# Optimization experiments

Hardware: AMD Instinct MI355X
Metric: run time of the kernel (lower is better)

The kernel has to match this reference:

```python
import jax, jax.numpy as jnp
import numpy as np

D_MODEL = 1024
N_HEADS = 16
N_KV_HEADS = 4
HEAD_DIM = D_MODEL // N_HEADS
NUM_REP = N_HEADS // N_KV_HEADS
B, T = 2, 2048


def setup_inputs() -> dict:
    key = jax.random.key(0)
    ks = jax.random.split(key, 9)
    s = 0.02
    x = jax.random.normal(ks[0], (B, T, D_MODEL), dtype=jnp.float32)
    # causal mask: True = masked (matches torch masked_fill semantics)
    mask = jnp.triu(jnp.ones((T, T), dtype=bool), k=1)[None, None]
    kv_dim = N_KV_HEADS * HEAD_DIM
    return {
        "x": x,
        "mask": mask,
        "Wq": jax.random.normal(ks[1], (D_MODEL, D_MODEL), jnp.float32) * s,
        "bq": jnp.zeros((D_MODEL,), jnp.float32),
        "Wk": jax.random.normal(ks[2], (D_MODEL, kv_dim), jnp.float32) * s,
        "bk": jnp.zeros((kv_dim,), jnp.float32),
        "Wv": jax.random.normal(ks[3], (D_MODEL, kv_dim), jnp.float32) * s,
        "bv": jnp.zeros((kv_dim,), jnp.float32),
        "Wo": jax.random.normal(ks[4], (D_MODEL, D_MODEL), jnp.float32) * s,
        "bo": jnp.zeros((D_MODEL,), jnp.float32),
    }


def reference(x, mask, Wq, bq, Wk, bk, Wv, bv, Wo, bo):
    Bx, Tx, C = x.shape
    # projections
    q = (x @ Wq + bq).reshape(Bx, Tx, N_HEADS, HEAD_DIM).transpose(0, 2, 1, 3)  # (B,H,T,D)
    k = (x @ Wk + bk).reshape(Bx, Tx, N_KV_HEADS, HEAD_DIM)
    v = (x @ Wv + bv).reshape(Bx, Tx, N_KV_HEADS, HEAD_DIM)
    # repeat_kv: expand+reshape == repeat along head axis
    k = jnp.repeat(k, NUM_REP, axis=2).transpose(0, 2, 1, 3)  # (B,H,T,D)
    v = jnp.repeat(v, NUM_REP, axis=2).transpose(0, 2, 1, 3)
    scale = 1.0 / jnp.sqrt(jnp.asarray(HEAD_DIM, x.dtype))
    attn = jnp.einsum('bhtd,bhsd->bhts', q, k) * scale  # (B,H,T,T)
    attn = jnp.where(mask, -jnp.inf, attn)
    attn = jax.nn.softmax(attn, axis=-1)
    out = jnp.einsum('bhts,bhsd->bhtd', attn, v)
    out = out.transpose(0, 2, 1, 3).reshape(Bx, Tx, C)
    return out @ Wo + bo
```

## Files before the change

kernel.cpp:

```cpp
#include <hip/hip_runtime.h>
#include <hip/hip_bf16.h>
#include <cmath>
#include <stdint.h>


typedef __attribute__((ext_vector_type(4))) float f32x4;
typedef __attribute__((ext_vector_type(16))) float f32x16;
typedef __attribute__((ext_vector_type(8))) short s16x8;
typedef __attribute__((ext_vector_type(8))) unsigned short u16x8;

#define MFMA16(a, b, c) __builtin_amdgcn_mfma_f32_16x16x32_bf16(a, b, c, 0, 0, 0)
#define MFMA32(a, b, c) __builtin_amdgcn_mfma_f32_32x32x16_bf16(a, b, c, 0, 0, 0)

__device__ __forceinline__ unsigned short f2bf(float f) {
    unsigned int u = __float_as_uint(f);
    u += 0x7FFFu + ((u >> 16) & 1u);
    return (unsigned short)(u >> 16);
}

__device__ __forceinline__ unsigned int pkbf(float lo, float hi) {
    return (unsigned int)f2bf(lo) | ((unsigned int)f2bf(hi) << 16);
}

__device__ __forceinline__ void async16(void* lds, const void* g) {
    __builtin_amdgcn_global_load_lds(
        (const __attribute__((address_space(1))) unsigned int*)g,
        (__attribute__((address_space(3))) unsigned int*)lds, 16, 0, 0);
}

__global__ __launch_bounds__(256) void prep(
        const float* __restrict__ x,
        const float* __restrict__ Wq, const float* __restrict__ Wk,
        const float* __restrict__ Wv, const float* __restrict__ Wo,
        const float* __restrict__ bq, const float* __restrict__ bk,
        const float* __restrict__ bv,
        unsigned short* __restrict__ xb, unsigned short* __restrict__ Wqkv,
        unsigned short* __restrict__ Wot, float* __restrict__ biasq, float qscale) {
    __shared__ float tile[32][33];
    const int bid = blockIdx.x, tid = threadIdx.x;
    if (bid < 2048) {
        const int id = bid * 256 + tid;
        const int row = id >> 7, kbf = id & 127;
        const float* src = x + (size_t)row * 1024 + kbf * 8;
        f32x4 lo = *reinterpret_cast<const f32x4*>(src);
        f32x4 hi = *reinterpret_cast<const f32x4*>(src + 4);
        u16x8 v = { f2bf(lo.x), f2bf(lo.y), f2bf(lo.z), f2bf(lo.w),
                    f2bf(hi.x), f2bf(hi.y), f2bf(hi.z), f2bf(hi.w) };
        const int mt = row >> 7, m = row & 127, kt = kbf >> 3, kb = kbf & 7;
        *reinterpret_cast<u16x8*>(&xb[(size_t)(((mt * 16 + kt) * 8 + kb) * 128 + m) * 8]) = v;
    } else if (bid < 4608) {
        int id = bid - 2048;
        const float* W; unsigned short* out; int N, nbase; float scale = 1.0f;
        if (id < 1024)      { W = Wq; out = Wqkv; N = 1024; nbase = 0;    scale = qscale; }
        else if (id < 1280) { W = Wk; out = Wqkv; N = 256;  nbase = 1024; id -= 1024; }
        else if (id < 1536) { W = Wv; out = Wqkv; N = 256;  nbase = 1280; id -= 1280; }
        else                { W = Wo; out = Wot;  N = 1024; nbase = 0;    id -= 1536; }
        const int nb = N >> 5;
        const int n0 = (id % nb) * 32, k0 = (id / nb) * 32;
        const int tx = tid & 31, ty = tid >> 5;
#pragma unroll
        for (int r = 0; r < 4; ++r)
            tile[ty + r * 8][tx] = W[(size_t)(k0 + ty + r * 8) * N + n0 + tx];
        __syncthreads();
        const int k = k0 + tx;
#pragma unroll
        for (int r = 0; r < 4; ++r) {
            const int n = nbase + n0 + ty + r * 8;
            size_t addr = (size_t)((n >> 7) * 16 + (k >> 6)) * 8192
                        + (size_t)((((k >> 3) & 7) * 128 + (n & 127)) * 8 + (k & 7));
            out[addr] = f2bf(tile[tx][ty + r * 8] * scale);
        }
    } else {
        const int i = (bid - 4608) * 256 + tid;
        if (i < 1024) biasq[i] = bq[i] * qscale;
        else if (i < 1280) biasq[i] = bk[i - 1024];
        else biasq[i] = bv[i - 1280];
    }
}

template <int EPI>
__global__ __launch_bounds__(256) void gemm128(
        const unsigned short* __restrict__ A, const unsigned short* __restrict__ Bt,
        const float* __restrict__ bias,
        unsigned short* __restrict__ oQ, unsigned short* __restrict__ oK,
        unsigned short* __restrict__ oV, float* __restrict__ oF) {
    __shared__ alignas(16) unsigned short sA[8 * 128 * 8];
    __shared__ alignas(16) unsigned short sB[8 * 128 * 8];
    const int tid = threadIdx.x;
    const int lane = tid & 63;
    const int ln = lane & 15, q = lane >> 4;
    const int w = tid >> 6;
    const int m0 = blockIdx.y * 128, n0 = blockIdx.x * 128;
    const int wm = (w & 1) * 64, wn = (w >> 1) * 64;

    f32x4 acc[4][4] = {};

    for (int kt = 0; kt < 16; ++kt) {
        const unsigned short* ab = A + ((size_t)(blockIdx.y * 16 + kt)) * 8192 + (size_t)tid * 8;
        const unsigned short* bb = Bt + ((size_t)(blockIdx.x * 16 + kt)) * 8192 + (size_t)tid * 8;
#pragma unroll
        for (int i = 0; i < 4; ++i)
            async16(&sA[(size_t)(i * 256 + (tid & 192)) * 8], ab + (size_t)i * 2048);
#pragma unroll
        for (int i = 0; i < 4; ++i)
            async16(&sB[(size_t)(i * 256 + (tid & 192)) * 8], bb + (size_t)i * 2048);
        __syncthreads();
#pragma unroll
        for (int kk = 0; kk < 2; ++kk) {
            const int kbq = (kk * 4 + q) * 128;
            s16x8 a[4], bfr[4];
#pragma unroll
            for (int mi = 0; mi < 4; ++mi)
                a[mi] = *reinterpret_cast<const s16x8*>(&sA[(size_t)(kbq + wm + mi * 16 + ln) * 8]);
#pragma unroll
            for (int ni = 0; ni < 4; ++ni)
                bfr[ni] = *reinterpret_cast<const s16x8*>(&sB[(size_t)(kbq + wn + ni * 16 + ln) * 8]);
#pragma unroll
            for (int mi = 0; mi < 4; ++mi)
#pragma unroll
                for (int ni = 0; ni < 4; ++ni)
                    acc[mi][ni] = MFMA16(a[mi], bfr[ni], acc[mi][ni]);
        }
        __syncthreads();
    }
#pragma unroll
    for (int ni = 0; ni < 4; ++ni) {
        const int col = n0 + wn + ni * 16 + ln;
        const float bv = bias[col];
#pragma unroll
        for (int mi = 0; mi < 4; ++mi) {
#pragma unroll
            for (int r = 0; r < 4; ++r) {
                const int row = m0 + wm + mi * 16 + q * 4 + r;
                const float v = acc[mi][ni][r] + bv;
                if (EPI == 0) {
                    if (col < 1024)      oQ[(size_t)row * 1024 + col] = f2bf(v);
                    else if (col < 1280) oK[(size_t)row * 256 + (col - 1024)] = f2bf(v);
                    else                 oV[(size_t)(col - 1280) * 4096 + row] = f2bf(v);
                } else {
                    oF[(size_t)row * 1024 + col] = v;
                }
            }
        }
    }
}

__global__ __launch_bounds__(256) void flash_attn(
        const unsigned short* __restrict__ Qb, const unsigned short* __restrict__ Kb,
        const unsigned short* __restrict__ Vt, unsigned short* __restrict__ Ot) {
    __shared__ alignas(16) unsigned short sK[64 * 72];
    __shared__ alignas(16) unsigned short sV[64 * 72];
    const int tid = threadIdx.x;
    const int lane = tid & 63, w = tid >> 6;
    const int ln = lane & 31, grp = lane >> 5;
    const int bh = blockIdx.x;
    const int yq = blockIdx.y;
    const int qt = (yq < 8) ? (15 - yq) : (yq - 8);
    const int b = bh >> 4, h = bh & 15, kvh = h >> 2;
    const int t0 = qt * 128;
    const int qrow_g = t0 + w * 32 + ln;

    const unsigned short* Qrow = Qb + (size_t)(b * 2048 + qrow_g) * 1024 + h * 64;
    s16x8 qf[4];
#pragma unroll
    for (int kk = 0; kk < 4; ++kk)
        qf[kk] = *reinterpret_cast<const s16x8*>(Qrow + kk * 16 + grp * 8);

    const unsigned short* Kbase = Kb + (size_t)(b * 2048) * 256 + kvh * 64;
    const unsigned short* Vbase = Vt + (size_t)(kvh * 64) * 4096 + (size_t)b * 2048;

    const int srow = tid >> 3, sd0 = (tid & 7) * 8;
    u16x8 kreg[2], vreg[2];
#pragma unroll
    for (int i = 0; i < 2; ++i) {
        kreg[i] = *reinterpret_cast<const u16x8*>(Kbase + (size_t)(srow + 32 * i) * 256 + sd0);
        vreg[i] = *reinterpret_cast<const u16x8*>(Vbase + (size_t)(srow + 32 * i) * 4096 + sd0);
    }

    f32x16 o0 = {}, o1 = {};
    float ltot = 0.f;
    const int nchunks = 2 * qt + 2;

    for (int c = 0; c < nchunks; ++c) {
        const int s0 = c * 64;
        __syncthreads();
#pragma unroll
        for (int i = 0; i < 2; ++i) {
            *reinterpret_cast<u16x8*>(&sK[(srow + 32 * i) * 72 + sd0]) = kreg[i];
            *reinterpret_cast<u16x8*>(&sV[(srow + 32 * i) * 72 + sd0]) = vreg[i];
        }
        __syncthreads();
        if (c + 1 < nchunks) {
            const int s1 = s0 + 64;
#pragma unroll
            for (int i = 0; i < 2; ++i) {
                kreg[i] = *reinterpret_cast<const u16x8*>(Kbase + (size_t)(s1 + srow + 32 * i) * 256 + sd0);
                vreg[i] = *reinterpret_cast<const u16x8*>(Vbase + (size_t)(srow + 32 * i) * 4096 + s1 + sd0);
            }
        }
        f32x16 st0 = {}, st1 = {};
#pragma unroll
        for (int kk = 0; kk < 4; ++kk) {
            s16x8 k0 = *reinterpret_cast<const s16x8*>(&sK[ln * 72 + kk * 16 + grp * 8]);
            s16x8 k1 = *reinterpret_cast<const s16x8*>(&sK[(32 + ln) * 72 + kk * 16 + grp * 8]);
            st0 = MFMA32(k0, qf[kk], st0);
            st1 = MFMA32(k1, qf[kk], st1);
        }
        if (s0 + 63 > t0 + w * 32) {
#pragma unroll
            for (int r = 0; r < 16; ++r) {
                const int keyo = s0 + (r & 3) + 8 * (r >> 2) + 4 * grp;
                if (keyo > qrow_g)      st0[r] = -INFINITY;
                if (keyo + 32 > qrow_g) st1[r] = -INFINITY;
            }
        }
        f32x16 p0, p1;
        float lsum = 0.f;
#pragma unroll
        for (int r = 0; r < 16; ++r) {
            p0[r] = __builtin_amdgcn_exp2f(st0[r]);
            p1[r] = __builtin_amdgcn_exp2f(st1[r]);
            lsum += p0[r] + p1[r];
        }
        ltot += lsum;
#pragma unroll
        for (int kkp = 0; kkp < 4; ++kkp) {
            const f32x16& pm = (kkp < 2) ? p0 : p1;
            const int A4 = 8 * (kkp & 1);
            unsigned int pA0 = pkbf(pm[A4 + 0], pm[A4 + 1]);
            unsigned int pA1 = pkbf(pm[A4 + 2], pm[A4 + 3]);
            unsigned int pB0 = pkbf(pm[A4 + 4], pm[A4 + 5]);
            unsigned int pB1 = pkbf(pm[A4 + 6], pm[A4 + 7]);
            unsigned int rA0 = (unsigned int)__shfl_xor((int)pA0, 32, 64);
            unsigned int rA1 = (unsigned int)__shfl_xor((int)pA1, 32, 64);
            unsigned int rB0 = (unsigned int)__shfl_xor((int)pB0, 32, 64);
            unsigned int rB1 = (unsigned int)__shfl_xor((int)pB1, 32, 64);
            union { unsigned int u[4]; s16x8 v; } pf;
            pf.u[0] = grp ? rB0 : pA0;
            pf.u[1] = grp ? rB1 : pA1;
            pf.u[2] = grp ? pB0 : rA0;
            pf.u[3] = grp ? pB1 : rA1;
            s16x8 v0 = *reinterpret_cast<const s16x8*>(&sV[ln * 72 + kkp * 16 + grp * 8]);
            s16x8 v1 = *reinterpret_cast<const s16x8*>(&sV[(32 + ln) * 72 + kkp * 16 + grp * 8]);
            o0 = MFMA32(pf.v, v0, o0);
            o1 = MFMA32(pf.v, v1, o1);
        }
    }

    const float lfull = ltot + __shfl_xor(ltot, 32, 64);
    const float rl = 1.0f / lfull;
    unsigned short* Otb = Ot + (size_t)((b * 16 + qt) * 16 + h) * 8192
                             + (size_t)(ln >> 3) * 1024 + (ln & 7);
#pragma unroll
    for (int r = 0; r < 16; ++r) {
        const int row = (r & 3) + 8 * (r >> 2) + 4 * grp;
        const float rr = __shfl(rl, row, 64);
        const size_t off = (size_t)(w * 32 + row) * 8;
        Otb[off]        = f2bf(o0[r] * rr);
        Otb[off + 4096] = f2bf(o1[r] * rr);
    }
}

extern "C" void kernel_launch(void* const* d_in, const int* in_sizes, int n_in,
                              void* d_out, int out_size, void* d_ws, size_t ws_size,
                              hipStream_t stream) {
    const float* x  = (const float*)d_in[0];
    const float* Wq = (const float*)d_in[2];
    const float* bq = (const float*)d_in[3];
    const float* Wk = (const float*)d_in[4];
    const float* bk = (const float*)d_in[5];
    const float* Wv = (const float*)d_in[6];
    const float* bv = (const float*)d_in[7];
    const float* Wo = (const float*)d_in[8];
    const float* bo = (const float*)d_in[9];
    float* out = (float*)d_out;

    char* ws = (char*)d_ws;
    unsigned short* xb    = (unsigned short*)(ws);
    unsigned short* Wqkv  = (unsigned short*)(ws + (8u  << 20));
    unsigned short* Wot   = (unsigned short*)(ws + (12u << 20));
    float*          biasq = (float*)         (ws + (15u << 20));
    unsigned short* Qb    = (unsigned short*)(ws + (16u << 20));
    unsigned short* Kb    = (unsigned short*)(ws + (24u << 20));
    unsigned short* Vtp   = (unsigned short*)(ws + (26u << 20));
    unsigned short* Otl   = (unsigned short*)(ws + (28u << 20));

    const float qscale = 0.125f * 1.4426950408889634f;

    prep<<<4614, 256, 0, stream>>>(x, Wq, Wk, Wv, Wo, bq, bk, bv,
                                   xb, Wqkv, Wot, biasq, qscale);
    gemm128<0><<<dim3(12, 32), 256, 0, stream>>>(xb, Wqkv, biasq, Qb, Kb, Vtp, nullptr);
    flash_attn<<<dim3(32, 16), 256, 0, stream>>>(Qb, Kb, Vtp, Otl);
    gemm128<1><<<dim3(8, 32), 256, 0, stream>>>(Otl, Wot, bo, nullptr, nullptr, nullptr, out);
}
```

Measured before the change: 199.5 us.

## Retile GEMMs to 128x64 with 32x32 MFMA, coalesce x prep, truncate P

Projection GEMMs now use 128x64 output tiles with 32x32x16 MFMA instructions, doubling the grid, and the weight layout is changed to 64-wide N blocks to match. The x-to-bf16 prep now stages 128x64 tiles through LDS so global writes become contiguous 16-byte stores. In attention, P is converted to bf16 by truncation through a byte-permute instead of round-to-nearest, and the row sum uses four partial accumulators. The grid changes trade per-block reuse for more parallelism, and truncation slightly lowers precision.

Measured after the change: 180.0 us. 1.11x faster.

```diff
diff --git a/kernel.cpp b/kernel.cpp
--- a/kernel.cpp
+++ b/kernel.cpp
@@ -9,7 +9,6 @@
 typedef __attribute__((ext_vector_type(8))) short s16x8;
 typedef __attribute__((ext_vector_type(8))) unsigned short u16x8;
 
-#define MFMA16(a, b, c) __builtin_amdgcn_mfma_f32_16x16x32_bf16(a, b, c, 0, 0, 0)
 #define MFMA32(a, b, c) __builtin_amdgcn_mfma_f32_32x32x16_bf16(a, b, c, 0, 0, 0)
 
 __device__ __forceinline__ unsigned short f2bf(float f) {
@@ -18,8 +17,8 @@
     return (unsigned short)(u >> 16);
 }
 
-__device__ __forceinline__ unsigned int pkbf(float lo, float hi) {
-    return (unsigned int)f2bf(lo) | ((unsigned int)f2bf(hi) << 16);
+__device__ __forceinline__ unsigned int pktr(float lo, float hi) {
+    return __builtin_amdgcn_perm(__float_as_uint(hi), __float_as_uint(lo), 0x07060302u);
 }
 
 __device__ __forceinline__ void async16(void* lds, const void* g) {
@@ -36,20 +35,31 @@
         const float* __restrict__ bv,
         unsigned short* __restrict__ xb, unsigned short* __restrict__ Wqkv,
         unsigned short* __restrict__ Wot, float* __restrict__ biasq, float qscale) {
+    __shared__ unsigned short sx[128 * 72];
     __shared__ float tile[32][33];
     const int bid = blockIdx.x, tid = threadIdx.x;
-    if (bid < 2048) {
-        const int id = bid * 256 + tid;
-        const int row = id >> 7, kbf = id & 127;
-        const float* src = x + (size_t)row * 1024 + kbf * 8;
-        f32x4 lo = *reinterpret_cast<const f32x4*>(src);
-        f32x4 hi = *reinterpret_cast<const f32x4*>(src + 4);
-        u16x8 v = { f2bf(lo.x), f2bf(lo.y), f2bf(lo.z), f2bf(lo.w),
-                    f2bf(hi.x), f2bf(hi.y), f2bf(hi.z), f2bf(hi.w) };
-        const int mt = row >> 7, m = row & 127, kt = kbf >> 3, kb = kbf & 7;
-        *reinterpret_cast<u16x8*>(&xb[(size_t)(((mt * 16 + kt) * 8 + kb) * 128 + m) * 8]) = v;
-    } else if (bid < 4608) {
-        int id = bid - 2048;
+    if (bid < 512) {
+        const int mt = bid >> 4, kt = bid & 15;
+#pragma unroll
+        for (int i = 0; i < 8; ++i) {
+            const int flat = (i * 256 + tid) * 4;
+            const int row = flat >> 6, col = flat & 63;
+            f32x4 ld = *reinterpret_cast<const f32x4*>(
+                &x[(size_t)(mt * 128 + row) * 1024 + kt * 64 + col]);
+            unsigned short* d = &sx[row * 72 + col];
+            d[0] = f2bf(ld.x); d[1] = f2bf(ld.y); d[2] = f2bf(ld.z); d[3] = f2bf(ld.w);
+        }
+        __syncthreads();
+#pragma unroll
+        for (int j = 0; j < 4; ++j) {
+            const int idx = j * 256 + tid;
+            const int kb = idx >> 7, m = idx & 127;
+            u16x8 v = *reinterpret_cast<const u16x8*>(&sx[m * 72 + kb * 8]);
+            *reinterpret_cast<u16x8*>(
+                &xb[(size_t)(((mt * 16 + kt) * 8 + kb) * 128 + m) * 8]) = v;
+        }
+    } else if (bid < 3072) {
+        int id = bid - 512;
         const float* W; unsigned short* out; int N, nbase; float scale = 1.0f;
         if (id < 1024)      { W = Wq; out = Wqkv; N = 1024; nbase = 0;    scale = qscale; }
         else if (id < 1280) { W = Wk; out = Wqkv; N = 256;  nbase = 1024; id -= 1024; }
@@ -66,12 +76,12 @@
 #pragma unroll
         for (int r = 0; r < 4; ++r) {
             const int n = nbase + n0 + ty + r * 8;
-            size_t addr = (size_t)((n >> 7) * 16 + (k >> 6)) * 8192
-                        + (size_t)((((k >> 3) & 7) * 128 + (n & 127)) * 8 + (k & 7));
+            size_t addr = (size_t)((n >> 6) * 16 + (k >> 6)) * 4096
+                        + (size_t)((((k >> 3) & 7) * 64 + (n & 63)) * 8 + (k & 7));
             out[addr] = f2bf(tile[tx][ty + r * 8] * scale);
         }
     } else {
-        const int i = (bid - 4608) * 256 + tid;
+        const int i = (bid - 3072) * 256 + tid;
         if (i < 1024) biasq[i] = bq[i] * qscale;
         else if (i < 1280) biasq[i] = bk[i - 1024];
         else biasq[i] = bv[i - 1280];
@@ -79,68 +89,61 @@
 }
 
 template <int EPI>
-__global__ __launch_bounds__(256) void gemm128(
+__global__ __launch_bounds__(256) void gemm_mn(
         const unsigned short* __restrict__ A, const unsigned short* __restrict__ Bt,
         const float* __restrict__ bias,
         unsigned short* __restrict__ oQ, unsigned short* __restrict__ oK,
         unsigned short* __restrict__ oV, float* __restrict__ oF) {
     __shared__ alignas(16) unsigned short sA[8 * 128 * 8];
-    __shared__ alignas(16) unsigned short sB[8 * 128 * 8];
+    __shared__ alignas(16) unsigned short sB[8 * 64 * 8];
     const int tid = threadIdx.x;
-    const int lane = tid & 63;
-    const int ln = lane & 15, q = lane >> 4;
-    const int w = tid >> 6;
-    const int m0 = blockIdx.y * 128, n0 = blockIdx.x * 128;
-    const int wm = (w & 1) * 64, wn = (w >> 1) * 64;
-
-    f32x4 acc[4][4] = {};
+    const int lane = tid & 63, w = tid >> 6;
+    const int l31 = lane & 31, grp = lane >> 5;
+    const int m0 = blockIdx.y * 128, n0 = blockIdx.x * 64;
+    const int wm = w * 32;
+
+    f32x16 acc0 = {}, acc1 = {};
 
     for (int kt = 0; kt < 16; ++kt) {
         const unsigned short* ab = A + ((size_t)(blockIdx.y * 16 + kt)) * 8192 + (size_t)tid * 8;
-        const unsigned short* bb = Bt + ((size_t)(blockIdx.x * 16 + kt)) * 8192 + (size_t)tid * 8;
+        const unsigned short* bb = Bt + ((size_t)(blockIdx.x * 16 + kt)) * 4096 + (size_t)tid * 8;
 #pragma unroll
         for (int i = 0; i < 4; ++i)
             async16(&sA[(size_t)(i * 256 + (tid & 192)) * 8], ab + (size_t)i * 2048);
 #pragma unroll
-        for (int i = 0; i < 4; ++i)
+        for (int i = 0; i < 2; ++i)
             async16(&sB[(size_t)(i * 256 + (tid & 192)) * 8], bb + (size_t)i * 2048);
         __syncthreads();
 #pragma unroll
-        for (int kk = 0; kk < 2; ++kk) {
-            const int kbq = (kk * 4 + q) * 128;
-            s16x8 a[4], bfr[4];
-#pragma unroll
-            for (int mi = 0; mi < 4; ++mi)
-                a[mi] = *reinterpret_cast<const s16x8*>(&sA[(size_t)(kbq + wm + mi * 16 + ln) * 8]);
-#pragma unroll
-            for (int ni = 0; ni < 4; ++ni)
-                bfr[ni] = *reinterpret_cast<const s16x8*>(&sB[(size_t)(kbq + wn + ni * 16 + ln) * 8]);
-#pragma unroll
-            for (int mi = 0; mi < 4; ++mi)
-#pragma unroll
-                for (int ni = 0; ni < 4; ++ni)
-                    acc[mi][ni] = MFMA16(a[mi], bfr[ni], acc[mi][ni]);
-        }
-        __syncthreads();
-    }
-#pragma unroll
-    for (int ni = 0; ni < 4; ++ni) {
-        const int col = n0 + wn + ni * 16 + ln;
-        const float bv = bias[col];
-#pragma unroll
-        for (int mi = 0; mi < 4; ++mi) {
-#pragma unroll
-            for (int r = 0; r < 4; ++r) {
-                const int row = m0 + wm + mi * 16 + q * 4 + r;
-                const float v = acc[mi][ni][r] + bv;
-                if (EPI == 0) {
-                    if (col < 1024)      oQ[(size_t)row * 1024 + col] = f2bf(v);
-                    else if (col < 1280) oK[(size_t)row * 256 + (col - 1024)] = f2bf(v);
-                    else                 oV[(size_t)(col - 1280) * 4096 + row] = f2bf(v);
-                } else {
-                    oF[(size_t)row * 1024 + col] = v;
-                }
+        for (int kc = 0; kc < 4; ++kc) {
+            const int kb = kc * 2 + grp;
+            s16x8 a  = *reinterpret_cast<const s16x8*>(&sA[(size_t)(kb * 128 + wm + l31) * 8]);
+            s16x8 b0 = *reinterpret_cast<const s16x8*>(&sB[(size_t)(kb * 64 + l31) * 8]);
+            s16x8 b1 = *reinterpret_cast<const s16x8*>(&sB[(size_t)(kb * 64 + 32 + l31) * 8]);
+            acc0 = MFMA32(a, b0, acc0);
+            acc1 = MFMA32(a, b1, acc1);
+        }
+        __syncthreads();
+    }
+    const float bv0 = bias[n0 + l31], bv1 = bias[n0 + 32 + l31];
+#pragma unroll
+    for (int r = 0; r < 16; ++r) {
+        const int row = m0 + wm + (r & 3) + 8 * (r >> 2) + 4 * grp;
+        const float v0 = acc0[r] + bv0, v1 = acc1[r] + bv1;
+        if (EPI == 0) {
+            if (n0 < 1024) {
+                oQ[(size_t)row * 1024 + n0 + l31] = f2bf(v0);
+                oQ[(size_t)row * 1024 + n0 + 32 + l31] = f2bf(v1);
+            } else if (n0 < 1280) {
+                oK[(size_t)row * 256 + (n0 - 1024) + l31] = f2bf(v0);
+                oK[(size_t)row * 256 + (n0 - 1024) + 32 + l31] = f2bf(v1);
+            } else {
+                oV[(size_t)(n0 - 1280 + l31) * 4096 + row] = f2bf(v0);
+                oV[(size_t)(n0 - 1280 + 32 + l31) * 4096 + row] = f2bf(v1);
             }
+        } else {
+            oF[(size_t)row * 1024 + n0 + l31] = v0;
+            oF[(size_t)row * 1024 + n0 + 32 + l31] = v1;
         }
     }
 }
@@ -215,22 +218,26 @@
             }
         }
         f32x16 p0, p1;
-        float lsum = 0.f;
 #pragma unroll
         for (int r = 0; r < 16; ++r) {
             p0[r] = __builtin_amdgcn_exp2f(st0[r]);
             p1[r] = __builtin_amdgcn_exp2f(st1[r]);
-            lsum += p0[r] + p1[r];
-        }
-        ltot += lsum;
+        }
+        float a0 = 0.f, a1 = 0.f, a2 = 0.f, a3 = 0.f;
+#pragma unroll
+        for (int r = 0; r < 16; r += 2) {
+            a0 += p0[r]; a1 += p0[r + 1];
+            a2 += p1[r]; a3 += p1[r + 1];
+        }
+        ltot += (a0 + a1) + (a2 + a3);
 #pragma unroll
         for (int kkp = 0; kkp < 4; ++kkp) {
             const f32x16& pm = (kkp < 2) ? p0 : p1;
             const int A4 = 8 * (kkp & 1);
-            unsigned int pA0 = pkbf(pm[A4 + 0], pm[A4 + 1]);
-            unsigned int pA1 = pkbf(pm[A4 + 2], pm[A4 + 3]);
-            unsigned int pB0 = pkbf(pm[A4 + 4], pm[A4 + 5]);
-            unsigned int pB1 = pkbf(pm[A4 + 6], pm[A4 + 7]);
+            unsigned int pA0 = pktr(pm[A4 + 0], pm[A4 + 1]);
+            unsigned int pA1 = pktr(pm[A4 + 2], pm[A4 + 3]);
+            unsigned int pB0 = pktr(pm[A4 + 4], pm[A4 + 5]);
+            unsigned int pB1 = pktr(pm[A4 + 6], pm[A4 + 7]);
             unsigned int rA0 = (unsigned int)__shfl_xor((int)pA0, 32, 64);
             unsigned int rA1 = (unsigned int)__shfl_xor((int)pA1, 32, 64);
             unsigned int rB0 = (unsigned int)__shfl_xor((int)pB0, 32, 64);
@@ -287,9 +294,9 @@
 
     const float qscale = 0.125f * 1.4426950408889634f;
 
-    prep<<<4614, 256, 0, stream>>>(x, Wq, Wk, Wv, Wo, bq, bk, bv,
+    prep<<<3078, 256, 0, stream>>>(x, Wq, Wk, Wv, Wo, bq, bk, bv,
                                    xb, Wqkv, Wot, biasq, qscale);
-    gemm128<0><<<dim3(12, 32), 256, 0, stream>>>(xb, Wqkv, biasq, Qb, Kb, Vtp, nullptr);
+    gemm_mn<0><<<dim3(24, 32), 256, 0, stream>>>(xb, Wqkv, biasq, Qb, Kb, Vtp, nullptr);
     flash_attn<<<dim3(32, 16), 256, 0, stream>>>(Qb, Kb, Vtp, Otl);
-    gemm128<1><<<dim3(8, 32), 256, 0, stream>>>(Otl, Wot, bo, nullptr, nullptr, nullptr, out);
-}
+    gemm_mn<1><<<dim3(16, 32), 256, 0, stream>>>(Otl, Wot, bo, nullptr, nullptr, nullptr, out);
+}
```
